# Optimization experiments

Hardware: AMD Instinct MI355X
Metric: run time of the kernel (lower is better)

Reference implementation:

```python
import jax, jax.numpy as jnp
import numpy as np

B, T, D, H, DH, M, L, OUT = 512, 49, 256, 8, 32, 1024, 4, 151
DI = H * DH
THR = 0.02


def _ln(x, g, b):
    mu = x.mean(-1, keepdims=True)
    v = ((x - mu) ** 2).mean(-1, keepdims=True)
    return (x - mu) / jnp.sqrt(v + 1e-5) * g + b


def setup_inputs() -> dict:
    key = jax.random.key(0)
    ks = iter(jax.random.split(key, 64))

    def W(*s):
        return jax.random.normal(next(ks), s, jnp.float32) * 0.02

    inp = {}
    for n in ['img0', 'img1', 'p0', 'p1', 'p2']:
        inp[n] = jax.random.normal(next(ks), (B, T, D), jnp.float32)
    inp['idx'] = jax.random.randint(next(ks), (3, 2, B, T), 0, T, dtype=jnp.int32)
    # two transformer encoders (image/point), stacked over [encoder=2, layer=L]
    inp['enc_ln1g'] = jnp.ones((2, L, D)); inp['enc_ln1b'] = jnp.zeros((2, L, D))
    inp['enc_wqkv'] = W(2, L, D, 3 * DI)
    inp['enc_wo'] = W(2, L, DI, D); inp['enc_bo'] = jnp.zeros((2, L, D))
    inp['enc_ln2g'] = jnp.ones((2, L, D)); inp['enc_ln2b'] = jnp.zeros((2, L, D))
    inp['enc_w1'] = W(2, L, D, M); inp['enc_b1'] = jnp.zeros((2, L, M))
    inp['enc_w2'] = W(2, L, M, D); inp['enc_b2'] = jnp.zeros((2, L, D))
    # per-depth score nets (PredictorLG)
    inp['sc_lng'] = jnp.ones((L, D)); inp['sc_lnb'] = jnp.zeros((L, D))
    inp['sc_w1'] = W(L, D, D); inp['sc_b1'] = jnp.zeros((L, D))
    inp['sc_w2'] = W(L, D, D // 2); inp['sc_b2'] = jnp.zeros((L, D // 2))
    inp['sc_w3'] = W(L, D // 2, 2); inp['sc_b3'] = jnp.zeros((L, 2))
    # per-depth patch MLPs (FFN dim->mlp_dim->mlp_dim->dim, 3 layers)
    inp['pm_w1'] = W(L, D, M); inp['pm_b1'] = jnp.zeros((L, M))
    inp['pm_w2'] = W(L, M, M); inp['pm_b2'] = jnp.zeros((L, M))
    inp['pm_w3'] = W(L, M, D); inp['pm_b3'] = jnp.zeros((L, D))
    # mlp head
    inp['hd_lng'] = jnp.ones((D,)); inp['hd_lnb'] = jnp.zeros((D,))
    inp['hd_w1'] = W(D, M); inp['hd_b1'] = jnp.zeros((M,))
    inp['hd_w2'] = W(M, OUT); inp['hd_b2'] = jnp.zeros((OUT,))
    return inp


def reference(img0, img1, p0, p1, p2, idx,
              enc_ln1g, enc_ln1b, enc_wqkv, enc_wo, enc_bo,
              enc_ln2g, enc_ln2b, enc_w1, enc_b1, enc_w2, enc_b2,
              sc_lng, sc_lnb, sc_w1, sc_b1, sc_w2, sc_b2, sc_w3, sc_b3,
              pm_w1, pm_b1, pm_w2, pm_b2, pm_w3, pm_b3,
              hd_lng, hd_lnb, hd_w1, hd_b1, hd_w2, hd_b2):

    def layer(x, e, i):
        # pre-norm attention
        h = _ln(x, enc_ln1g[e, i], enc_ln1b[e, i])
        qkv = h @ enc_wqkv[e, i]                      # [B,T,3*DI]
        q, k, v = jnp.split(qkv, 3, axis=-1)
        q = q.reshape(B, T, H, DH); k = k.reshape(B, T, H, DH); v = v.reshape(B, T, H, DH)
        a = jax.nn.softmax(jnp.einsum('bqhd,bkhd->bhqk', q, k) * (DH ** -0.5), -1)
        o = jnp.einsum('bhqk,bkhd->bqhd', a, v).reshape(B, T, DI)
        x = x + o @ enc_wo[e, i] + enc_bo[e, i]
        # pre-norm FFN
        h = _ln(x, enc_ln2g[e, i], enc_ln2b[e, i])
        return x + jax.nn.gelu(h @ enc_w1[e, i] + enc_b1[e, i]) @ enc_w2[e, i] + enc_b2[e, i]

    image_feats = [img0, img1]
    point_feats = [p0, p1, p2]
    pred_scores = []
    for i in range(L):
        image_tokens = [layer(f, 0, i) for f in image_feats]
        point_tokens = [layer(f, 1, i) for f in point_feats]
        allt = jnp.concatenate(image_tokens + point_tokens, axis=1)  # [B, 5*T, D]
        h = _ln(allt, sc_lng[i], sc_lnb[i])
        h = jax.nn.gelu(h @ sc_w1[i] + sc_b1[i])
        h = jax.nn.gelu(h @ sc_w2[i] + sc_b2[i])
        scores = jax.nn.softmax(h @ sc_w3[i] + sc_b3[i], -1)[:, :, 0]  # [B, 5*T]
        pred_scores.append(scores)
        mask = (scores > THR).astype(jnp.int32)[..., None]            # [B,5*T,1]
        fm = mask.astype(allt.dtype)
        fnm = (-mask - 1).astype(allt.dtype)  # torch ~int_mask is bitwise NOT: ~1=-2, ~0=-1 (faithful)
        image_feats = [image_tokens[j] * fm[:, j * T:(j + 1) * T]
                       + image_tokens[1 - j] * fnm[:, j * T:(j + 1) * T] for j in range(2)]

        def patch_mlp(x):
            h2 = jax.nn.gelu(x @ pm_w1[i] + pm_b1[i])
            h2 = jax.nn.gelu(h2 @ pm_w2[i] + pm_b2[i])
            return h2 @ pm_w3[i] + pm_b3[i]

        new_p = []
        for k2 in range(3):
            s0 = 2 * T + k2 * T
            g0 = jnp.take_along_axis(image_tokens[0], idx[k2, 0][..., None], axis=1)
            g1 = jnp.take_along_axis(image_tokens[1], idx[k2, 1][..., None], axis=1)
            patch = patch_mlp(g0) + patch_mlp(g1)
            new_p.append(point_tokens[k2] * fm[:, s0:s0 + T] + patch * fnm[:, s0:s0 + T])
        point_feats = new_p

    pooled = jnp.concatenate(image_feats + point_feats, axis=1).max(axis=1)  # [B, D]
    h = _ln(pooled, hd_lng, hd_lnb)
    smplx = jax.nn.gelu(h @ hd_w1 + hd_b1) @ hd_w2 + hd_b2                   # [B, OUT]
    pred_score = jnp.concatenate(pred_scores, axis=1)                         # [B, L*5*T]
    return smplx, pred_score
```

## Files before the change

### kernel.cpp

```cpp
#include <hip/hip_runtime.h>
#include <math.h>

#define B_ 512
#define T_ 49
#define D_ 256
#define M_ 1024
#define L_ 4
#define OUT_ 151
#define BT_ 25088
#define NTOK5 (5*BT_)
#define THRESH 0.02f

typedef __bf16 bf16x8 __attribute__((ext_vector_type(8)));
typedef float f32x4 __attribute__((ext_vector_type(4)));
typedef unsigned short us;

__device__ __forceinline__ float gelu_t(float x){
    float u = 0.7978845608028654f * x * (1.0f + 0.044715f*x*x);
    float e = __expf(-2.0f*u);
    return __fdividef(x, 1.0f + e);
}
__device__ __forceinline__ us f2bf(float f){
    unsigned int u = __float_as_uint(f);
    u += 0x7fffu + ((u>>16)&1u);
    return (us)(u>>16);
}
__device__ __forceinline__ float bf2f(us h){
    return __uint_as_float(((unsigned int)h)<<16);
}
__device__ __forceinline__ void gload16(const void* g, void* l){
    __builtin_amdgcn_global_load_lds(
        (const __attribute__((address_space(1))) void*)g,
        (__attribute__((address_space(3))) void*)l, 16, 0, 0);
}

__global__ void copy_in_kernel(const float* __restrict__ a0, const float* __restrict__ a1,
                               const float* __restrict__ a2, const float* __restrict__ a3,
                               const float* __restrict__ a4, float* __restrict__ dst){
    size_t i = (size_t)blockIdx.x*256 + threadIdx.x;
    if (i >= (size_t)NTOK5*64) return;
    int slot = (int)(i / ((size_t)BT_*64));
    size_t off = i % ((size_t)BT_*64);
    const float* src = slot==0?a0: slot==1?a1: slot==2?a2: slot==3?a3: a4;
    ((float4*)dst)[i] = ((const float4*)src)[off];
}

__global__ void xcvt_kernel(const float* __restrict__ x, us* __restrict__ y, int nrows){
    size_t i = (size_t)blockIdx.x*256 + threadIdx.x;
    if (i >= (size_t)nrows*64) return;
    float4 v = ((const float4*)x)[i];
    ushort4 o; o.x=f2bf(v.x); o.y=f2bf(v.y); o.z=f2bf(v.z); o.w=f2bf(v.w);
    ((ushort4*)y)[i] = o;
}

template<bool OBF>
__global__ void ln_kernel(const float* __restrict__ x, const float* __restrict__ g,
                          const float* __restrict__ b, void* __restrict__ y, int nrows){
    int row = blockIdx.x*4 + (threadIdx.x>>6);
    if (row >= nrows) return;
    int lane = threadIdx.x & 63;
    float4 v = ((const float4*)(x + (size_t)row*D_))[lane];
    float s  = v.x+v.y+v.z+v.w;
    float sq = v.x*v.x + v.y*v.y + v.z*v.z + v.w*v.w;
    #pragma unroll
    for (int o=32;o;o>>=1){ s += __shfl_xor(s,o,64); sq += __shfl_xor(sq,o,64); }
    float mu = s*(1.0f/256.0f);
    float rstd = rsqrtf(sq*(1.0f/256.0f) - mu*mu + 1e-5f);
    float4 gv = ((const float4*)g)[lane];
    float4 bv = ((const float4*)b)[lane];
    float o0 = (v.x-mu)*rstd*gv.x + bv.x;
    float o1 = (v.y-mu)*rstd*gv.y + bv.y;
    float o2 = (v.z-mu)*rstd*gv.z + bv.z;
    float o3 = (v.w-mu)*rstd*gv.w + bv.w;
    if (OBF){
        ushort4 o4; o4.x=f2bf(o0); o4.y=f2bf(o1); o4.z=f2bf(o2); o4.w=f2bf(o3);
        ((ushort4*)((us*)y + (size_t)row*D_))[lane] = o4;
    } else {
        float4 o4; o4.x=o0; o4.y=o1; o4.z=o2; o4.w=o3;
        ((float4*)((float*)y + (size_t)row*D_))[lane] = o4;
    }
}

__global__ void wtrans_kernel(const float* __restrict__ W, us* __restrict__ Wt,
                              int K, int N){
    int g = blockIdx.z;
    __shared__ float t[32][33];
    int k0 = blockIdx.y*32, n0 = blockIdx.x*32;
    int tx = threadIdx.x&31, ty = threadIdx.x>>5;
    for (int r=ty; r<32; r+=8){
        int k = k0+r, n = n0+tx;
        t[r][tx] = (k<K && n<N) ? W[(size_t)g*K*N + (size_t)k*N + n] : 0.f;
    }
    __syncthreads();
    for (int r=ty; r<32; r+=8){
        int n = n0+r, k = k0+tx;
        if (n<N && k<K) Wt[(size_t)g*N*K + (size_t)n*K + k] = f2bf(t[tx][r]);
    }
}

__global__ void wtrans_pad_kernel(const float* __restrict__ W, us* __restrict__ Wt,
                                  int K, int Nsrc, int Ndst){
    __shared__ float t[32][33];
    int k0 = blockIdx.y*32, n0 = blockIdx.x*32;
    int tx = threadIdx.x&31, ty = threadIdx.x>>5;
    for (int r=ty; r<32; r+=8){
        int k = k0+r, n = n0+tx;
        t[r][tx] = (k<K && n<Nsrc) ? W[(size_t)k*Nsrc + n] : 0.f;
    }
    __syncthreads();
    for (int r=ty; r<32; r+=8){
        int n = n0+r, k = k0+tx;
        if (n<Ndst && k<K) Wt[(size_t)n*K + k] = f2bf(t[tx][r]);
    }
}

__global__ void padb_kernel(const float* __restrict__ b, float* __restrict__ o,
                            int Nsrc, int Ndst){
    int i = blockIdx.x*256 + threadIdx.x;
    if (i < Ndst) o[i] = (i < Nsrc) ? b[i] : 0.f;
}

__global__ void headcopy_kernel(const float* __restrict__ src, float* __restrict__ dst){
    int i = blockIdx.x*256 + threadIdx.x;
    if (i >= B_*OUT_) return;
    int r = i / OUT_, c = i % OUT_;
    dst[i] = src[(size_t)r*256 + c];
}

__device__ __forceinline__ void gemm_compute(const us* As, const us* Bs,
        int wr, int wc, int lr, int kg, f32x4 (&acc)[4][4]){
    bf16x8 av[4], bv[4];
    #pragma unroll
    for (int mi=0;mi<4;mi++){
        int r = wr*64 + mi*16 + lr;
        av[mi] = *(const bf16x8*)(&As[r*32 + ((kg ^ ((r>>1)&3))<<3)]);
    }
    #pragma unroll
    for (int ni=0;ni<4;ni++){
        int c = wc*64 + ni*16 + lr;
        bv[ni] = *(const bf16x8*)(&Bs[c*32 + ((kg ^ ((c>>1)&3))<<3)]);
    }
    #pragma unroll
    for (int mi=0;mi<4;mi++)
        #pragma unroll
        for (int ni=0;ni<4;ni++)
            acc[mi][ni] = __builtin_amdgcn_mfma_f32_16x16x32_bf16(av[mi], bv[ni], acc[mi][ni], 0, 0, 0);
}

template<int ACT, int RIN, bool OBF>
__global__ __launch_bounds__(256) void mfma_gemm(
    const us* __restrict__ A, const us* __restrict__ Wt,
    const float* __restrict__ bias, const void* __restrict__ resid,
    void* __restrict__ Cout, int Mr, int N, int K)
{
    __shared__ __align__(16) us SM[2*8192];
    const int nwg  = gridDim.x*gridDim.y;
    const int flat = blockIdx.y*gridDim.x + blockIdx.x;
    const int qq = nwg>>3, rr = nwg&7;
    const int xcd = flat&7, sidx = flat>>3;
    const int logical = (xcd<rr) ? (xcd*(qq+1)+sidx) : (rr*(qq+1)+(xcd-rr)*qq+sidx);
    const int bn = (logical % gridDim.x)*128;
    const int bm = (logical / gridDim.x)*128;
    const int tid = threadIdx.x;
    const int lane = tid&63, w = tid>>6;
    const int wr = w>>1, wc = w&1;
    const int lr = lane&15, kg = lane>>4;
    f32x4 acc[4][4] = {};

    const int j0 = tid, j1 = tid+256;
    const int row0 = j0>>2, row1 = j1>>2;
    const int k8s0 = (j0&3) ^ ((row0>>1)&3);
    const int k8s1 = (j1&3) ^ ((row1>>1)&3);
    int ga0 = bm+row0; if (ga0>=Mr) ga0=Mr-1;
    int ga1 = bm+row1; if (ga1>=Mr) ga1=Mr-1;
    int gb0 = bn+row0; if (gb0>=N) gb0=N-1;
    int gb1 = bn+row1; if (gb1>=N) gb1=N-1;
    const us* a0p = A  + (size_t)ga0*K + k8s0*8;
    const us* a1p = A  + (size_t)ga1*K + k8s1*8;
    const us* b0p = Wt + (size_t)gb0*K + k8s0*8;
    const us* b1p = Wt + (size_t)gb1*K + k8s1*8;

    const int nk = K >> 5;
    {
        us* b0 = SM;
        gload16(a0p, b0 + j0*8);
        gload16(a1p, b0 + j1*8);
        gload16(b0p, b0 + 4096 + j0*8);
        gload16(b1p, b0 + 4096 + j1*8);
        us* b1 = SM + 8192;
        gload16(a0p+32, b1 + j0*8);
        gload16(a1p+32, b1 + j1*8);
        gload16(b0p+32, b1 + 4096 + j0*8);
        gload16(b1p+32, b1 + 4096 + j1*8);
    }
    int cur = 0;
    for (int t=0; t<nk-1; ++t){
        asm volatile("s_waitcnt vmcnt(4)" ::: "memory");
        __builtin_amdgcn_s_barrier();
        __builtin_amdgcn_sched_barrier(0);
        const us* cbase = SM + cur*8192;
        gemm_compute(cbase, cbase+4096, wr, wc, lr, kg, acc);
        __builtin_amdgcn_sched_barrier(0);
        __builtin_amdgcn_s_barrier();
        if (t+2 < nk){
            us* nbase = SM + cur*8192;
            int k0 = (t+2)<<5;
            gload16(a0p+k0, nbase + j0*8);
            gload16(a1p+k0, nbase + j1*8);
            gload16(b0p+k0, nbase + 4096 + j0*8);
            gload16(b1p+k0, nbase + 4096 + j1*8);
        }
        cur ^= 1;
    }
    asm volatile("s_waitcnt vmcnt(0)" ::: "memory");
    __builtin_amdgcn_s_barrier();
    __builtin_amdgcn_sched_barrier(0);
    {
        const us* cbase = SM + cur*8192;
        gemm_compute(cbase, cbase+4096, wr, wc, lr, kg, acc);
    }
    __syncthreads();

    if (OBF && RIN==0){
        us* Cs16 = (us*)SM;
        #pragma unroll
        for (int mi=0;mi<4;mi++){
            #pragma unroll
            for (int ni=0;ni<4;ni++){
                #pragma unroll
                for (int r4=0;r4<4;r4++){
                    int row = wr*64 + mi*16 + kg*4 + r4;
                    int col = wc*64 + ni*16 + lr;
                    float v = acc[mi][ni][r4];
                    if (bias) v += bias[bn + col];
                    if (ACT==1) v = gelu_t(v);
                    int h = ((row>>2)&3) | ((row&1)<<2);
                    int punit = (col>>3) ^ h;
                    Cs16[row*128 + punit*8 + (col&7)] = f2bf(v);
                }
            }
        }
        __syncthreads();
        {
            int rbase = tid>>3, seg = tid&7;
            #pragma unroll
            for (int pass=0; pass<8; ++pass){
                int row = rbase + (pass>>1)*32;
                int half = pass&1;
                int grow = bm + row;
                if (grow < Mr){
                    int h = ((row>>2)&3) | ((row&1)<<2);
                    int punit = (half*8+seg) ^ h;
                    *(uint4*)((us*)Cout + (size_t)grow*N + bn + half*64 + seg*8)
                        = *(const uint4*)&Cs16[row*128 + punit*8];
                }
            }
        }
        return;
    }

    float* Cs = (float*)SM;
    #pragma unroll
    for (int er=0; er<2; er++){
        #pragma unroll
        for (int ml=0; ml<2; ml++){
            int mi = er*2 + ml;
            #pragma unroll
            for (int ni=0;ni<4;ni++){
                #pragma unroll
                for (int r4=0;r4<4;r4++){
                    int lrow = wr*32 + ml*16 + kg*4 + r4;
                    int lcol = wc*64 + ni*16 + lr;
                    int pcol = lcol ^ (((lrow>>2)&1)<<4);
                    float v = acc[mi][ni][r4];
                    if (bias) v += bias[bn + lcol];
                    if (ACT==1) v = gelu_t(v);
                    Cs[lrow*128 + pcol] = v;
                }
            }
        }
        __syncthreads();
        #pragma unroll
        for (int s=0; s<2; s++){
            int lrow = (tid>>3) + s*32;
            int tseg = tid&7;
            int pseg = tseg ^ ((lrow>>2)&1);
            const float4* src = (const float4*)&Cs[lrow*128 + pseg*16];
            float4 v0=src[0], v1=src[1], v2=src[2], v3=src[3];
            int grow = bm + (lrow>>5)*64 + (er*2 + ((lrow>>4)&1))*16 + (lrow&15);
            int gcol = bn + tseg*16;
            if (grow < Mr){
                if (RIN==1){
                    const float4* rp = (const float4*)((const float*)resid + (size_t)grow*N + gcol);
                    float4 r0=rp[0], r1=rp[1], r2=rp[2], r3=rp[3];
                    v0.x+=r0.x; v0.y+=r0.y; v0.z+=r0.z; v0.w+=r0.w;
                    v1.x+=r1.x; v1.y+=r1.y; v1.z+=r1.z; v1.w+=r1.w;
                    v2.x+=r2.x; v2.y+=r2.y; v2.z+=r2.z; v2.w+=r2.w;
                    v3.x+=r3.x; v3.y+=r3.y; v3.z+=r3.z; v3.w+=r3.w;
                } else if (RIN==2){
                    const uint4* rp = (const uint4*)((const us*)resid + (size_t)grow*N + gcol);
                    uint4 u0=rp[0], u1=rp[1];
                    v0.x+=bf2f((us)(u0.x&0xffff)); v0.y+=bf2f((us)(u0.x>>16));
                    v0.z+=bf2f((us)(u0.y&0xffff)); v0.w+=bf2f((us)(u0.y>>16));
                    v1.x+=bf2f((us)(u0.z&0xffff)); v1.y+=bf2f((us)(u0.z>>16));
                    v1.z+=bf2f((us)(u0.w&0xffff)); v1.w+=bf2f((us)(u0.w>>16));
                    v2.x+=bf2f((us)(u1.x&0xffff)); v2.y+=bf2f((us)(u1.x>>16));
                    v2.z+=bf2f((us)(u1.y&0xffff)); v2.w+=bf2f((us)(u1.y>>16));
                    v3.x+=bf2f((us)(u1.z&0xffff)); v3.y+=bf2f((us)(u1.z>>16));
                    v3.z+=bf2f((us)(u1.w&0xffff)); v3.w+=bf2f((us)(u1.w>>16));
                }
                if (OBF){
                    unsigned int w0 = (unsigned)f2bf(v0.x) | ((unsigned)f2bf(v0.y)<<16);
                    unsigned int w1 = (unsigned)f2bf(v0.z) | ((unsigned)f2bf(v0.w)<<16);
                    unsigned int w2 = (unsigned)f2bf(v1.x) | ((unsigned)f2bf(v1.y)<<16);
                    unsigned int w3 = (unsigned)f2bf(v1.z) | ((unsigned)f2bf(v1.w)<<16);
                    unsigned int w4 = (unsigned)f2bf(v2.x) | ((unsigned)f2bf(v2.y)<<16);
                    unsigned int w5 = (unsigned)f2bf(v2.z) | ((unsigned)f2bf(v2.w)<<16);
                    unsigned int w6 = (unsigned)f2bf(v3.x) | ((unsigned)f2bf(v3.y)<<16);
                    unsigned int w7 = (unsigned)f2bf(v3.z) | ((unsigned)f2bf(v3.w)<<16);
                    uint4* op = (uint4*)((us*)Cout + (size_t)grow*N + gcol);
                    uint4 u0; u0.x=w0; u0.y=w1; u0.z=w2; u0.w=w3;
                    uint4 u1; u1.x=w4; u1.y=w5; u1.z=w6; u1.w=w7;
                    op[0]=u0; op[1]=u1;
                } else {
                    float4* op = (float4*)((float*)Cout + (size_t)grow*N + gcol);
                    op[0]=v0; op[1]=v1; op[2]=v2; op[3]=v3;
                }
            }
        }
        __syncthreads();
    }
}

__global__ __launch_bounds__(128) void attn_kernel(const us* __restrict__ qkv,
                                                   us* __restrict__ o){
    __shared__ float ks[2][T_][36], vs[2][T_][36];
    const int w = threadIdx.x >> 6, lane = threadIdx.x & 63;
    const int bh = blockIdx.x*2 + w;
    const int bb = bh >> 3, h = bh & 7;
    const us* base = qkv + (size_t)bb*T_*768 + h*32;
    if (lane < T_){
        const uint4* kp = (const uint4*)(base + (size_t)lane*768 + 256);
        const uint4* vp = (const uint4*)(base + (size_t)lane*768 + 512);
        #pragma unroll
        for (int j=0;j<4;j++){
            uint4 ku = kp[j], vu = vp[j];
            unsigned ka[4]={ku.x,ku.y,ku.z,ku.w}, va[4]={vu.x,vu.y,vu.z,vu.w};
            #pragma unroll
            for (int e=0;e<4;e++){
                ks[w][lane][j*8+e*2]   = bf2f((us)(ka[e]&0xffffu));
                ks[w][lane][j*8+e*2+1] = bf2f((us)(ka[e]>>16));
                vs[w][lane][j*8+e*2]   = bf2f((us)(va[e]&0xffffu));
                vs[w][lane][j*8+e*2+1] = bf2f((us)(va[e]>>16));
            }
        }
    }
    __syncthreads();
    if (lane >= T_) return;
    float q[32];
    {
        const uint4* qp = (const uint4*)(base + (size_t)lane*768);
        #pragma unroll
        for (int j=0;j<4;j++){
            uint4 qu = qp[j];
            unsigned qa[4]={qu.x,qu.y,qu.z,qu.w};
            #pragma unroll
            for (int e=0;e<4;e++){
                q[j*8+e*2]   = bf2f((us)(qa[e]&0xffffu));
                q[j*8+e*2+1] = bf2f((us)(qa[e]>>16));
            }
        }
    }
    float S[T_];
    #pragma unroll
    for (int c=0;c<T_;c++){
        float acc = 0.f;
        #pragma unroll
        for (int d=0;d<32;d++) acc += q[d]*ks[w][c][d];
        S[c] = acc*0.17677669529663687f;
    }
    float m = S[0];
    #pragma unroll
    for (int c=1;c<T_;c++) m = fmaxf(m, S[c]);
    float sum = 0.f;
    #pragma unroll
    for (int c=0;c<T_;c++){ S[c] = __expf(S[c]-m); sum += S[c]; }
    float inv = __fdividef(1.f, sum);
    float oa[32];
    #pragma unroll
    for (int d=0;d<32;d++) oa[d] = 0.f;
    #pragma unroll
    for (int c=0;c<T_;c++){
        float p2 = S[c]*inv;
        #pragma unroll
        for (int d=0;d<32;d++) oa[d] += p2*vs[w][c][d];
    }
    unsigned* op = (unsigned*)(o + ((size_t)bb*T_ + lane)*256 + h*32);
    #pragma unroll
    for (int j=0;j<16;j++)
        op[j] = (unsigned)f2bf(oa[2*j]) | ((unsigned)f2bf(oa[2*j+1])<<16);
}

__global__ void score_kernel(const us* __restrict__ s2, const float* __restrict__ w3,
                             const float* __restrict__ b3, float* __restrict__ sc,
                             float* __restrict__ pred, int layer, int row0, int nrows){
    int lr = blockIdx.x*256 + threadIdx.x;
    if (lr >= nrows) return;
    int row = row0 + lr;
    int s = row / BT_;
    int r = row % BT_;
    int b = r / T_;
    int t = r % T_;
    const uint4* xv = (const uint4*)(s2 + (size_t)lr*128);
    float l0 = b3[0], l1 = b3[1];
    #pragma unroll
    for (int q=0;q<16;q++){
        uint4 u = xv[q];
        unsigned int uu[4] = {u.x,u.y,u.z,u.w};
        #pragma unroll
        for (int e=0;e<4;e++){
            float fa = bf2f((us)(uu[e]&0xffff));
            float fb = bf2f((us)(uu[e]>>16));
            int d = q*8 + e*2;
            l0 += fa*w3[d*2]     + fb*w3[(d+1)*2];
            l1 += fa*w3[d*2+1]   + fb*w3[(d+1)*2+1];
        }
    }
    float m = fmaxf(l0,l1);
    float e0 = __expf(l0-m), e1 = __expf(l1-m);
    float sc0 = __fdividef(e0, e0+e1);
    sc[b*(5*T_) + s*T_ + t] = sc0;
    pred[(size_t)b*(L_*5*T_) + (size_t)layer*(5*T_) + s*T_ + t] = sc0;
}

__global__ void img_fuse_kernel(float* __restrict__ X, const float* __restrict__ sc){
    size_t i = (size_t)blockIdx.x*256 + threadIdx.x;
    if (i >= (size_t)BT_*64) return;
    int row = (int)(i>>6), d4 = (int)(i&63);
    int b = row / T_, t = row % T_;
    float s0 = sc[b*(5*T_) + t];
    float s1 = sc[b*(5*T_) + T_ + t];
    float fm0  = (s0 > THRESH)? 1.f : 0.f;
    float fnm0 = -fm0 - 1.f;
    float fm1  = (s1 > THRESH)? 1.f : 0.f;
    float fnm1 = -fm1 - 1.f;
    float4* p0 = ((float4*)(X + (size_t)row*D_)) + d4;
    float4* p1 = ((float4*)(X + ((size_t)BT_ + row)*D_)) + d4;
    float4 a0 = *p0, a1 = *p1;
    float4 r0, r1;
    r0.x = a0.x*fm0 + a1.x*fnm0;  r0.y = a0.y*fm0 + a1.y*fnm0;
    r0.z = a0.z*fm0 + a1.z*fnm0;  r0.w = a0.w*fm0 + a1.w*fnm0;
    r1.x = a1.x*fm1 + a0.x*fnm1;  r1.y = a1.y*fm1 + a0.y*fnm1;
    r1.z = a1.z*fm1 + a0.z*fnm1;  r1.w = a1.w*fm1 + a0.w*fnm1;
    *p0 = r0; *p1 = r1;
}

__global__ void pt_fuse_gather_kernel(float* __restrict__ X, const us* __restrict__ PM,
                                      const int* __restrict__ idx, const float* __restrict__ sc){
    size_t i = (size_t)blockIdx.x*256 + threadIdx.x;
    if (i >= (size_t)3*BT_*64) return;
    int vrow = (int)(i>>6), d4 = (int)(i&63);
    int k2 = vrow / BT_, grow = vrow % BT_;
    int b = grow / T_, t = grow % T_;
    float s = sc[b*(5*T_) + (2+k2)*T_ + t];
    float fm  = (s > THRESH)? 1.f : 0.f;
    float fnm = -fm - 1.f;
    int i0 = idx[(size_t)(k2*2+0)*BT_ + grow];
    int i1 = idx[(size_t)(k2*2+1)*BT_ + grow];
    uint2 u0 = ((const uint2*)(PM + ((size_t)b*T_ + i0)*D_))[d4];
    uint2 u1 = ((const uint2*)(PM + ((size_t)BT_ + (size_t)b*T_ + i1)*D_))[d4];
    float p0 = bf2f((us)(u0.x&0xffff)) + bf2f((us)(u1.x&0xffff));
    float p1 = bf2f((us)(u0.x>>16))    + bf2f((us)(u1.x>>16));
    float p2 = bf2f((us)(u0.y&0xffff)) + bf2f((us)(u1.y&0xffff));
    float p3 = bf2f((us)(u0.y>>16))    + bf2f((us)(u1.y>>16));
    float4* xp = ((float4*)(X + ((size_t)(2+k2)*BT_ + grow)*D_)) + d4;
    float4 a = *xp;
    float4 rr;
    rr.x = a.x*fm + p0*fnm;
    rr.y = a.y*fm + p1*fnm;
    rr.z = a.z*fm + p2*fnm;
    rr.w = a.w*fm + p3*fnm;
    *xp = rr;
}

__global__ void pool_kernel(const float* __restrict__ x, float* __restrict__ p){
    int i = blockIdx.x*256 + threadIdx.x;
    if (i >= B_*64) return;
    int b = i>>6, d4 = i&63;
    float4 m; m.x=m.y=m.z=m.w=-3.4e38f;
    for (int s=0;s<5;s++){
        const float4* bp = ((const float4*)(x + ((size_t)s*BT_ + (size_t)b*T_)*D_)) + d4;
        for (int t=0;t<T_;t++){
            float4 v = bp[(size_t)t*64];
            m.x=fmaxf(m.x,v.x); m.y=fmaxf(m.y,v.y); m.z=fmaxf(m.z,v.z); m.w=fmaxf(m.w,v.w);
        }
    }
    ((float4*)p)[i] = m;
}

static inline int cdiv(int a, int b){ return (a+b-1)/b; }

extern "C" void kernel_launch(void* const* d_in, const int* in_sizes, int n_in,
                              void* d_out, int out_size, void* d_ws, size_t ws_size,
                              hipStream_t stream)
{
    const float* in_img0 = (const float*)d_in[0];
    const float* in_img1 = (const float*)d_in[1];
    const float* in_p0   = (const float*)d_in[2];
    const float* in_p1   = (const float*)d_in[3];
    const float* in_p2   = (const float*)d_in[4];
    const int*   in_idx  = (const int*)d_in[5];
    const float* enc_ln1g = (const float*)d_in[6];
    const float* enc_ln1b = (const float*)d_in[7];
    const float* enc_wqkv = (const float*)d_in[8];
    const float* enc_wo   = (const float*)d_in[9];
    const float* enc_bo   = (const float*)d_in[10];
    const float* enc_ln2g = (const float*)d_in[11];
    const float* enc_ln2b = (const float*)d_in[12];
    const float* enc_w1   = (const float*)d_in[13];
    const float* enc_b1   = (const float*)d_in[14];
    const float* enc_w2   = (const float*)d_in[15];
    const float* enc_b2   = (const float*)d_in[16];
    const float* sc_lng   = (const float*)d_in[17];
    const float* sc_lnb   = (const float*)d_in[18];
    const float* sc_w1    = (const float*)d_in[19];
    const float* sc_b1    = (const float*)d_in[20];
    const float* sc_w2    = (const float*)d_in[21];
    const float* sc_b2    = (const float*)d_in[22];
    const float* sc_w3    = (const float*)d_in[23];
    const float* sc_b3    = (const float*)d_in[24];
    const float* pm_w1    = (const float*)d_in[25];
    const float* pm_b1    = (const float*)d_in[26];
    const float* pm_w2    = (const float*)d_in[27];
    const float* pm_b2    = (const float*)d_in[28];
    const float* pm_w3    = (const float*)d_in[29];
    const float* pm_b3    = (const float*)d_in[30];
    const float* hd_lng   = (const float*)d_in[31];
    const float* hd_lnb   = (const float*)d_in[32];
    const float* hd_w1    = (const float*)d_in[33];
    const float* hd_b1    = (const float*)d_in[34];
    const float* hd_w2    = (const float*)d_in[35];
    const float* hd_b2    = (const float*)d_in[36];

    char* p = (char*)d_ws;
    float* X   = (float*)p;  p += (size_t)5*BT_*D_*4;
    float* SCb = (float*)p;  p += (size_t)B_*5*T_*4;
    us* PM   = (us*)p; p += (size_t)2*BT_*D_*2;
    us* WQKV = (us*)p; p += (size_t)8*768*256*2;
    us* WWO  = (us*)p; p += (size_t)8*256*256*2;
    us* WW1  = (us*)p; p += (size_t)8*1024*256*2;
    us* WW2  = (us*)p; p += (size_t)8*256*1024*2;
    us* WS1  = (us*)p; p += (size_t)4*256*256*2;
    us* WS2  = (us*)p; p += (size_t)4*128*256*2;
    us* WP1  = (us*)p; p += (size_t)4*1024*256*2;
    us* WP2  = (us*)p; p += (size_t)4*1024*1024*2;
    us* WP3  = (us*)p; p += (size_t)4*256*1024*2;
    us* WH1  = (us*)p; p += (size_t)1024*256*2;
    us* WH2  = (us*)p; p += (size_t)256*1024*2;
    float* B2P  = (float*)p; p += (size_t)256*4;
    float* POOL = (float*)p; p += (size_t)B_*256*4;
    us*    HLNb = (us*)p;  p += (size_t)B_*256*2;
    us*    HMIDb= (us*)p;  p += (size_t)B_*1024*2;
    float* HOUT = (float*)p; p += (size_t)B_*256*4;
    size_t fixed = (size_t)(p - (char*)d_ws);
    long long poolb = (long long)ws_size - (long long)fixed;
    if (poolb < 0) poolb = 0;
    auto chunkOf = [&](long long perRow, int maxRows)->int{
        long long c = poolb / perRow;
        c = (c / T_) * T_;
        if (c < T_) c = T_;
        if (c > maxRows) c = maxRows;
        return (int)c;
    };
    auto evenC = [&](int total, int Cmax)->int{
        int nch = (total + Cmax - 1)/Cmax;
        int per = (total + nch - 1)/nch;
        per = ((per + T_ - 1)/T_)*T_;
        if (per > Cmax) per = Cmax;
        return per;
    };
    int CencMax = chunkOf(2560, 3*BT_);
    int CscMax  = chunkOf(1024, NTOK5);
    int CpmMax  = chunkOf(4096, 2*BT_);
    char* pb = p;
    us* eR1 = (us*)pb;
    us* eR2 = (us*)(pb + (size_t)CencMax*512);
    us* eR3 = eR1;
    us* sR1 = (us*)pb;
    us* sS1 = (us*)(pb + (size_t)CscMax*512);
    us* sS2 = sR1;
    us* m1  = (us*)pb;
    us* m2  = (us*)(pb + (size_t)CpmMax*2048);
    us* cA  = m2;

    float* out_smplx = (float*)d_out;
    float* out_pred  = out_smplx + (size_t)B_*OUT_;

    wtrans_kernel<<<dim3(cdiv(768,32), cdiv(256,32), 8),256,0,stream>>>(enc_wqkv, WQKV, 256, 768);
    wtrans_kernel<<<dim3(cdiv(256,32), cdiv(256,32), 8),256,0,stream>>>(enc_wo,   WWO,  256, 256);
    wtrans_kernel<<<dim3(cdiv(1024,32),cdiv(256,32), 8),256,0,stream>>>(enc_w1,   WW1,  256, 1024);
    wtrans_kernel<<<dim3(cdiv(256,32), cdiv(1024,32),8),256,0,stream>>>(enc_w2,   WW2,  1024,256);
    wtrans_kernel<<<dim3(cdiv(256,32), cdiv(256,32), 4),256,0,stream>>>(sc_w1,    WS1,  256, 256);
    wtrans_kernel<<<dim3(cdiv(128,32), cdiv(256,32), 4),256,0,stream>>>(sc_w2,    WS2,  256, 128);
    wtrans_kernel<<<dim3(cdiv(1024,32),cdiv(256,32), 4),256,0,stream>>>(pm_w1,    WP1,  256, 1024);
    wtrans_kernel<<<dim3(cdiv(1024,32),cdiv(1024,32),4),256,0,stream>>>(pm_w2,    WP2,  1024,1024);
    wtrans_kernel<<<dim3(cdiv(256,32), cdiv(1024,32),4),256,0,stream>>>(pm_w3,    WP3,  1024,256);
    wtrans_kernel<<<dim3(cdiv(1024,32),cdiv(256,32), 1),256,0,stream>>>(hd_w1,    WH1,  256, 1024);
    wtrans_pad_kernel<<<dim3(cdiv(256,32), cdiv(1024,32)),256,0,stream>>>(hd_w2, WH2, 1024, 151, 256);
    padb_kernel<<<1,256,0,stream>>>(hd_b2, B2P, 151, 256);

    copy_in_kernel<<<cdiv(NTOK5*64,256), 256, 0, stream>>>(in_img0,in_img1,in_p0,in_p1,in_p2, X);

    for (int i=0;i<L_;i++){
        for (int grp=0; grp<2; grp++){
            int base  = (grp==0)? 0 : 2*BT_;
            int total = (grp==0)? 2*BT_ : 3*BT_;
            size_t wi = (size_t)(grp*L_ + i);
            int C = evenC(total, CencMax);
            for (int off=0; off<total; off+=C){
                int R = total-off < C ? total-off : C;
                float* Xp = X + (size_t)(base+off)*D_;
                ln_kernel<true><<<cdiv(R,4),256,0,stream>>>(Xp, enc_ln1g+wi*D_, enc_ln1b+wi*D_, eR1, R);
                mfma_gemm<0,0,true><<<dim3(6, cdiv(R,128)),256,0,stream>>>(
                    eR1, WQKV + wi*768*256, nullptr, nullptr, eR2, R, 768, 256);
                attn_kernel<<<(R/T_)*4,128,0,stream>>>(eR2, eR3);
                mfma_gemm<0,1,false><<<dim3(2, cdiv(R,128)),256,0,stream>>>(
                    eR3, WWO + wi*256*256, enc_bo + wi*D_, Xp, Xp, R, 256, 256);
                ln_kernel<true><<<cdiv(R,4),256,0,stream>>>(Xp, enc_ln2g+wi*D_, enc_ln2b+wi*D_, eR1, R);
                mfma_gemm<1,0,true><<<dim3(8, cdiv(R,128)),256,0,stream>>>(
                    eR1, WW1 + wi*1024*256, enc_b1 + wi*M_, nullptr, eR2, R, 1024, 256);
                mfma_gemm<0,1,false><<<dim3(2, cdiv(R,128)),256,0,stream>>>(
                    eR2, WW2 + wi*256*1024, enc_b2 + wi*D_, Xp, Xp, R, 256, 1024);
            }
        }
        {
            int C = evenC(NTOK5, CscMax);
            for (int off=0; off<NTOK5; off+=C){
                int R = NTOK5-off < C ? NTOK5-off : C;
                ln_kernel<true><<<cdiv(R,4),256,0,stream>>>(X + (size_t)off*D_,
                    sc_lng+(size_t)i*D_, sc_lnb+(size_t)i*D_, sR1, R);
                mfma_gemm<1,0,true><<<dim3(2, cdiv(R,128)),256,0,stream>>>(
                    sR1, WS1 + (size_t)i*256*256, sc_b1+(size_t)i*D_, nullptr, sS1, R, 256, 256);
                mfma_gemm<1,0,true><<<dim3(1, cdiv(R,128)),256,0,stream>>>(
                    sS1, WS2 + (size_t)i*128*256, sc_b2+(size_t)i*128, nullptr, sS2, R, 128, 256);
                score_kernel<<<cdiv(R,256),256,0,stream>>>(
                    sS2, sc_w3+(size_t)i*256, sc_b3+(size_t)i*2, SCb, out_pred, i, off, R);
            }
        }
        {
            int C = evenC(2*BT_, CpmMax);
            for (int off=0; off<2*BT_; off+=C){
                int R = 2*BT_-off < C ? 2*BT_-off : C;
                xcvt_kernel<<<cdiv(R*64,256),256,0,stream>>>(X + (size_t)off*D_, cA, R);
                mfma_gemm<1,0,true><<<dim3(8, cdiv(R,128)),256,0,stream>>>(
                    cA, WP1 + (size_t)i*1024*256, pm_b1+(size_t)i*M_, nullptr, m1, R, 1024, 256);
                mfma_gemm<1,0,true><<<dim3(8, cdiv(R,128)),256,0,stream>>>(
                    m1, WP2 + (size_t)i*1024*1024, pm_b2+(size_t)i*M_, nullptr, m2, R, 1024, 1024);
                mfma_gemm<0,0,true><<<dim3(2, cdiv(R,128)),256,0,stream>>>(
                    m2, WP3 + (size_t)i*256*1024, pm_b3+(size_t)i*D_, nullptr, PM + (size_t)off*D_, R, 256, 1024);
            }
        }
        pt_fuse_gather_kernel<<<cdiv(3*BT_*64,256),256,0,stream>>>(X, PM, in_idx, SCb);
        img_fuse_kernel<<<cdiv(BT_*64,256),256,0,stream>>>(X, SCb);
    }
    pool_kernel<<<cdiv(B_*64,256),256,0,stream>>>(X, POOL);
    ln_kernel<true><<<cdiv(B_,4),256,0,stream>>>(POOL, hd_lng, hd_lnb, HLNb, B_);
    mfma_gemm<1,0,true><<<dim3(8, cdiv(B_,128)),256,0,stream>>>(
        HLNb, WH1, hd_b1, nullptr, HMIDb, B_, 1024, 256);
    mfma_gemm<0,0,false><<<dim3(2, cdiv(B_,128)),256,0,stream>>>(
        HMIDb, WH2, B2P, nullptr, HOUT, B_, 256, 1024);
    headcopy_kernel<<<cdiv(B_*OUT_,256),256,0,stream>>>(HOUT, out_smplx);
}
```

Baseline: 6.089 ms.

## Use triple-buffered LDS in MFMA GEMM to drop the second barrier per k-step

```diff
diff --git a/kernel.cpp b/kernel.cpp
--- a/kernel.cpp
+++ b/kernel.cpp
@@ -153,7 +153,7 @@
     const float* __restrict__ bias, const void* __restrict__ resid,
     void* __restrict__ Cout, int Mr, int N, int K)
 {
-    __shared__ __align__(16) us SM[2*8192];
+    __shared__ __align__(16) us SM[3*8192];
     const int nwg  = gridDim.x*gridDim.y;
     const int flat = blockIdx.y*gridDim.x + blockIdx.x;
     const int qq = nwg>>3, rr = nwg&7;
@@ -181,44 +181,22 @@
     const us* b1p = Wt + (size_t)gb1*K + k8s1*8;
 
     const int nk = K >> 5;
-    {
-        us* b0 = SM;
-        gload16(a0p, b0 + j0*8);
-        gload16(a1p, b0 + j1*8);
-        gload16(b0p, b0 + 4096 + j0*8);
-        gload16(b1p, b0 + 4096 + j1*8);
-        us* b1 = SM + 8192;
-        gload16(a0p+32, b1 + j0*8);
-        gload16(a1p+32, b1 + j1*8);
-        gload16(b0p+32, b1 + 4096 + j0*8);
-        gload16(b1p+32, b1 + 4096 + j1*8);
-    }
-    int cur = 0;
-    for (int t=0; t<nk-1; ++t){
-        asm volatile("s_waitcnt vmcnt(4)" ::: "memory");
+    #define STAGEK(t_) { us* nb_ = SM + ((t_)%3)*8192; int k0_ = (t_)<<5; \
+        gload16(a0p + k0_, nb_ + j0*8); \
+        gload16(a1p + k0_, nb_ + j1*8); \
+        gload16(b0p + k0_, nb_ + 4096 + j0*8); \
+        gload16(b1p + k0_, nb_ + 4096 + j1*8); }
+    STAGEK(0); STAGEK(1);
+    for (int t=0; t<nk; ++t){
+        if (t+1 < nk) asm volatile("s_waitcnt vmcnt(4)" ::: "memory");
+        else          asm volatile("s_waitcnt vmcnt(0)" ::: "memory");
         __builtin_amdgcn_s_barrier();
         __builtin_amdgcn_sched_barrier(0);
-        const us* cbase = SM + cur*8192;
-        gemm_compute(cbase, cbase+4096, wr, wc, lr, kg, acc);
-        __builtin_amdgcn_sched_barrier(0);
-        __builtin_amdgcn_s_barrier();
-        if (t+2 < nk){
-            us* nbase = SM + cur*8192;
-            int k0 = (t+2)<<5;
-            gload16(a0p+k0, nbase + j0*8);
-            gload16(a1p+k0, nbase + j1*8);
-            gload16(b0p+k0, nbase + 4096 + j0*8);
-            gload16(b1p+k0, nbase + 4096 + j1*8);
-        }
-        cur ^= 1;
-    }
-    asm volatile("s_waitcnt vmcnt(0)" ::: "memory");
-    __builtin_amdgcn_s_barrier();
-    __builtin_amdgcn_sched_barrier(0);
-    {
-        const us* cbase = SM + cur*8192;
-        gemm_compute(cbase, cbase+4096, wr, wc, lr, kg, acc);
-    }
+        if (t+2 < nk) STAGEK(t+2);
+        const us* cb = SM + (t%3)*8192;
+        gemm_compute(cb, cb+4096, wr, wc, lr, kg, acc);
+    }
+    #undef STAGEK
     __syncthreads();
 
     if (OBF && RIN==0){
```

New measurement: 6.092 ms. About the same (+0.1%).
